# Performance work log

Measured on AMD Instinct MI355X. Metric: run time of the kernel, lower is better.

The kernel has to match this reference:

```python
import jax, jax.numpy as jnp
import numpy as np

D_MODEL = 4096
N_CHUNKS = 8
CHUNK = D_MODEL // N_CHUNKS
EPS = 1e-5


def setup_inputs() -> dict:
    key = jax.random.key(0)
    k = jax.random.split(key, 5)
    B, L = 4, 4096
    x = jax.random.normal(k[0], (B, L, D_MODEL), dtype=jnp.float32)
    # kaiming_uniform with a=sqrt(5) on [n,c,c]: fan_in = c, bound = 1/sqrt(fan_in)
    bound = 1.0 / np.sqrt(CHUNK)
    w1 = jax.random.uniform(k[1], (N_CHUNKS, CHUNK, CHUNK), jnp.float32, -bound, bound)
    w2 = jax.random.uniform(k[2], (N_CHUNKS, CHUNK, CHUNK), jnp.float32, -bound, bound)
    b1 = jnp.zeros((N_CHUNKS, CHUNK), jnp.float32)
    b2 = jnp.zeros((N_CHUNKS, CHUNK), jnp.float32)
    ln_g = jnp.ones((D_MODEL,), jnp.float32)
    ln_b = jnp.zeros((D_MODEL,), jnp.float32)
    return {"x": x, "w1": w1, "b1": b1, "w2": w2, "b2": b2, "ln_g": ln_g, "ln_b": ln_b}


def reference(x, w1, b1, w2, b2, ln_g, ln_b):
    B, L, d = x.shape
    xc = x.reshape(B, L, N_CHUNKS, CHUNK)
    h = jnp.einsum('blnc,ncd->blnd', xc, w1) + b1
    h = jax.nn.gelu(h, approximate=False)  # torch F.gelu default is exact erf
    h = jnp.einsum('blnc,ncd->blnd', h, w2) + b2
    out = h.reshape(B, L, d) + x  # dropout p=0.0 -> identity
    mu = jnp.mean(out, axis=-1, keepdims=True)
    var = jnp.var(out, axis=-1, keepdims=True)
    return (out - mu) * jax.lax.rsqrt(var + EPS) * ln_g + ln_b
```

## Files before the change

kernel.cpp:

```cpp
#include <hip/hip_runtime.h>
#include <hip/hip_bf16.h>

#define TOKENS 16384
#define DMODEL 4096
#define NCH 8
#define CH 512
#define BM 64

typedef short s16x8 __attribute__((ext_vector_type(8)));
typedef float f32x4 __attribute__((ext_vector_type(4)));

__device__ __forceinline__ unsigned short f2bf(float f) {
    unsigned u = __float_as_uint(f);
    u += 0x7fffu + ((u >> 16) & 1u);
    return (unsigned short)(u >> 16);
}

__device__ __forceinline__ float gelu_fast(float x) {
    float u = 1.5957691216057308f * x * (1.0f + 0.044715f * x * x);
    float e = __expf(u);
    return x - x * __builtin_amdgcn_rcpf(e + 1.0f);
}

__global__ __launch_bounds__(256)
void wprep_kernel(const float* __restrict__ w1, const float* __restrict__ w2,
                  unsigned short* __restrict__ p1, unsigned short* __restrict__ p2)
{
    const int lane = threadIdx.x;
    const int sub  = threadIdx.y;
    const int kt   = blockIdx.x;
    const int nb   = blockIdx.y * 4 + sub;
    const int which = blockIdx.z >> 3;
    const int n     = blockIdx.z & 7;

    const int kg  = lane >> 4;
    const int l15 = lane & 15;

    const float* src = (which ? w2 : w1) + (size_t)n * CH * CH;
    unsigned short* dst = (which ? p2 : p1) + (size_t)n * CH * CH
                        + ((size_t)(kt * 32 + nb) * 64 + lane) * 8;

    unsigned short v[8];
#pragma unroll
    for (int j = 0; j < 8; ++j)
        v[j] = f2bf(src[(size_t)(kt * 32 + kg * 8 + j) * CH + nb * 16 + l15]);

    uint4 q;
    q.x = (unsigned)v[0] | ((unsigned)v[1] << 16);
    q.y = (unsigned)v[2] | ((unsigned)v[3] << 16);
    q.z = (unsigned)v[4] | ((unsigned)v[5] << 16);
    q.w = (unsigned)v[6] | ((unsigned)v[7] << 16);
    *(uint4*)dst = q;
}

template<int BDEPTH>
__device__ __forceinline__ void gemm_half(
    const unsigned short* __restrict__ wp,
    const unsigned char* lds,
    int nbase,
    int lane, int l15, int kg,
    f32x4 (&acc)[4][4])
{
    s16x8 B[BDEPTH][4], A[2][4];
    auto loadB = [&](int buf, int kt) {
        const unsigned short* p = wp + ((size_t)(kt * 32 + nbase) * 64 + lane) * 8;
#pragma unroll
        for (int ni = 0; ni < 4; ++ni)
            B[buf][ni] = *(const s16x8*)(p + (size_t)ni * 64 * 8);
    };
    auto loadA = [&](int buf, int kt) {
#pragma unroll
        for (int mi = 0; mi < 4; ++mi) {
            int r = mi * 16 + l15;
            int byte = ((r * CH + kt * 32 + kg * 8) * 2) ^ ((r & 7) << 4);
            A[buf][mi] = *(const s16x8*)(lds + byte);
        }
    };

#pragma unroll
    for (int i = 0; i < BDEPTH; ++i) loadB(i, i);
    loadA(0, 0);

#pragma unroll
    for (int k = 0; k < 16; ++k) {
        if (k < 15) loadA((k + 1) & 1, k + 1);
        __builtin_amdgcn_s_setprio(1);
#pragma unroll
        for (int ni = 0; ni < 4; ++ni)
#pragma unroll
            for (int mi = 0; mi < 4; ++mi)
                acc[mi][ni] = __builtin_amdgcn_mfma_f32_16x16x32_bf16(
                    A[k & 1][mi], B[k % BDEPTH][ni], acc[mi][ni], 0, 0, 0);
        __builtin_amdgcn_s_setprio(0);
        if (k < 16 - BDEPTH) loadB(k % BDEPTH, k + BDEPTH);
    }
}

__global__ __launch_bounds__(256, 2)
void mlp_kernel(const float* __restrict__ x,
                const unsigned short* __restrict__ p1,
                const unsigned short* __restrict__ p2,
                const float* __restrict__ b1,
                const float* __restrict__ b2,
                float* __restrict__ mid)
{
    __shared__ unsigned char lds[BM * CH * 2];
    const int tile = blockIdx.x;
    const int n    = blockIdx.y;
    const int tid  = threadIdx.x;
    const int wid  = tid >> 6;
    const int lane = tid & 63;
    const int row0 = tile * BM;

    {
        const float* xc = x + (size_t)row0 * DMODEL + n * CH;
#pragma unroll
        for (int it = 0; it < 32; ++it) {
            int f = it * 256 + tid;
            int r = f >> 7;
            int c = (f & 127) << 2;
            const float4 v = *(const float4*)(xc + (size_t)r * DMODEL + c);
            unsigned lo = (unsigned)f2bf(v.x) | ((unsigned)f2bf(v.y) << 16);
            unsigned hi = (unsigned)f2bf(v.z) | ((unsigned)f2bf(v.w) << 16);
            int byte = ((r * CH + c) * 2) ^ ((r & 7) << 4);
            *(uint2*)(lds + byte) = make_uint2(lo, hi);
        }
    }
    __syncthreads();

    const int nwoff = wid * 128;
    const int l15   = lane & 15;
    const int kg    = lane >> 4;

    float b1v[8], b2v[8];
#pragma unroll
    for (int h = 0; h < 2; ++h)
#pragma unroll
        for (int ni = 0; ni < 4; ++ni) {
            int col = n * CH + nwoff + h * 64 + ni * 16 + l15;
            b1v[h * 4 + ni] = b1[col];
            b2v[h * 4 + ni] = b2[col];
        }

    const unsigned short* p1n = p1 + (size_t)n * CH * CH;
    const unsigned short* p2n = p2 + (size_t)n * CH * CH;

    f32x4 acc[4][4];
    auto zacc = [&]() {
#pragma unroll
        for (int mi = 0; mi < 4; ++mi)
#pragma unroll
            for (int ni = 0; ni < 4; ++ni)
                acc[mi][ni] = (f32x4){0.f, 0.f, 0.f, 0.f};
    };

    zacc();
    gemm_half<3>(p1n, lds, wid * 8 + 0, lane, l15, kg, acc);

    unsigned g0[4][4][2];
#pragma unroll
    for (int mi = 0; mi < 4; ++mi)
#pragma unroll
        for (int ni = 0; ni < 4; ++ni)
#pragma unroll
            for (int j = 0; j < 2; ++j) {
                float v0 = gelu_fast(acc[mi][ni][2 * j]     + b1v[ni]);
                float v1 = gelu_fast(acc[mi][ni][2 * j + 1] + b1v[ni]);
                g0[mi][ni][j] = (unsigned)f2bf(v0) | ((unsigned)f2bf(v1) << 16);
            }

    zacc();
    gemm_half<2>(p1n, lds, wid * 8 + 4, lane, l15, kg, acc);

    __syncthreads();

#pragma unroll
    for (int mi = 0; mi < 4; ++mi)
#pragma unroll
        for (int ni = 0; ni < 4; ++ni)
#pragma unroll
            for (int j = 0; j < 2; ++j) {
                int col  = nwoff + ni * 16 + l15;
                int row  = mi * 16 + kg * 4 + 2 * j;
                int byte0 = ((row * CH + col) * 2) ^ ((row & 7) << 4);
                *(unsigned short*)(lds + byte0) = (unsigned short)(g0[mi][ni][j] & 0xffff);
                int row1 = row + 1;
                int byte1 = ((row1 * CH + col) * 2) ^ ((row1 & 7) << 4);
                *(unsigned short*)(lds + byte1) = (unsigned short)(g0[mi][ni][j] >> 16);
            }
#pragma unroll
    for (int mi = 0; mi < 4; ++mi)
#pragma unroll
        for (int ni = 0; ni < 4; ++ni)
#pragma unroll
            for (int r = 0; r < 4; ++r) {
                float v = gelu_fast(acc[mi][ni][r] + b1v[4 + ni]);
                int col  = nwoff + 64 + ni * 16 + l15;
                int row  = mi * 16 + kg * 4 + r;
                int byte = ((row * CH + col) * 2) ^ ((row & 7) << 4);
                *(unsigned short*)(lds + byte) = f2bf(v);
            }
    __syncthreads();

    const float* xr = x   + (size_t)row0 * DMODEL + n * CH;
    float*       mr = mid + (size_t)row0 * DMODEL + n * CH;

#pragma unroll
    for (int h = 0; h < 2; ++h) {
        zacc();
        if (h == 0) gemm_half<3>(p2n, lds, wid * 8 + 0, lane, l15, kg, acc);
        else        gemm_half<3>(p2n, lds, wid * 8 + 4, lane, l15, kg, acc);
#pragma unroll
        for (int mi = 0; mi < 4; ++mi)
#pragma unroll
            for (int ni = 0; ni < 4; ++ni)
#pragma unroll
                for (int r = 0; r < 4; ++r) {
                    int row = mi * 16 + kg * 4 + r;
                    int col = nwoff + h * 64 + ni * 16 + l15;
                    float v = acc[mi][ni][r] + b2v[h * 4 + ni] + xr[(size_t)row * DMODEL + col];
                    mr[(size_t)row * DMODEL + col] = v;
                }
    }
}

__global__ __launch_bounds__(256)
void ln_kernel(float* __restrict__ out,
               const float* __restrict__ g,
               const float* __restrict__ bt)
{
    __shared__ float red[8];
    const int row = blockIdx.x;
    const int tid = threadIdx.x;
    float* p = out + (size_t)row * DMODEL;

    float4 v[4];
    float s = 0.f, ss = 0.f;
#pragma unroll
    for (int i = 0; i < 4; ++i) {
        v[i] = *(const float4*)(p + (i * 256 + tid) * 4);
        s  += v[i].x + v[i].y + v[i].z + v[i].w;
        ss += v[i].x * v[i].x + v[i].y * v[i].y + v[i].z * v[i].z + v[i].w * v[i].w;
    }
#pragma unroll
    for (int o = 32; o > 0; o >>= 1) {
        s  += __shfl_xor(s, o, 64);
        ss += __shfl_xor(ss, o, 64);
    }
    const int wid = tid >> 6, lane = tid & 63;
    if (lane == 0) { red[wid] = s; red[4 + wid] = ss; }
    __syncthreads();
    s  = red[0] + red[1] + red[2] + red[3];
    ss = red[4] + red[5] + red[6] + red[7];
    const float mu   = s * (1.f / DMODEL);
    const float var  = ss * (1.f / DMODEL) - mu * mu;
    const float rstd = rsqrtf(var + 1e-5f);

#pragma unroll
    for (int i = 0; i < 4; ++i) {
        int c = (i * 256 + tid) * 4;
        float4 gv = *(const float4*)(g + c);
        float4 bv = *(const float4*)(bt + c);
        float4 o;
        o.x = (v[i].x - mu) * rstd * gv.x + bv.x;
        o.y = (v[i].y - mu) * rstd * gv.y + bv.y;
        o.z = (v[i].z - mu) * rstd * gv.z + bv.z;
        o.w = (v[i].w - mu) * rstd * gv.w + bv.w;
        *(float4*)(p + c) = o;
    }
}

extern "C" void kernel_launch(void* const* d_in, const int* in_sizes, int n_in,
                              void* d_out, int out_size, void* d_ws, size_t ws_size,
                              hipStream_t stream)
{
    const float* x    = (const float*)d_in[0];
    const float* w1   = (const float*)d_in[1];
    const float* b1   = (const float*)d_in[2];
    const float* w2   = (const float*)d_in[3];
    const float* b2   = (const float*)d_in[4];
    const float* ln_g = (const float*)d_in[5];
    const float* ln_b = (const float*)d_in[6];
    float* out = (float*)d_out;

    unsigned short* p1 = (unsigned short*)d_ws;
    unsigned short* p2 = p1 + (size_t)NCH * CH * CH;

    wprep_kernel<<<dim3(16, 8, 16), dim3(64, 4), 0, stream>>>(w1, w2, p1, p2);
    mlp_kernel<<<dim3(TOKENS / BM, NCH), dim3(256), 0, stream>>>(x, p1, p2, b1, b2, out);
    ln_kernel<<<dim3(TOKENS), dim3(256), 0, stream>>>(out, ln_g, ln_b);
}
```

Before: 363.1 us.

## Shrink row tile to 32 and use 8 waves each owning a 64-column slice

The MLP kernel tile drops from 64 to 32 rows and the block grows from 256 to 512 threads, so each of the 8 waves computes a 32x64 output slice in one pass instead of two 64-column halves. The GEMM helper uses double-buffered B and A loads in place of the deeper B prefetch, and the s_setprio hints are removed. LDS use halves and there are twice as many blocks, which may raise occupancy and shrink per-thread register pressure. The cost is that each block reads the full weight chunk from global/L2 for half as many rows, doubling weight traffic per token, and the per-step MFMA count drops, which gives less room to hide load latency.

Result: slower. 450.3 us (+24.0%).

```diff
diff --git a/kernel.cpp b/kernel.cpp
--- a/kernel.cpp
+++ b/kernel.cpp
@@ -5,7 +5,7 @@
 #define DMODEL 4096
 #define NCH 8
 #define CH 512
-#define BM 64
+#define BM 32
 
 typedef short s16x8 __attribute__((ext_vector_type(8)));
 typedef float f32x4 __attribute__((ext_vector_type(4)));
@@ -53,50 +53,44 @@
     *(uint4*)dst = q;
 }
 
-template<int BDEPTH>
-__device__ __forceinline__ void gemm_half(
+__device__ __forceinline__ void gemm_pass(
     const unsigned short* __restrict__ wp,
     const unsigned char* lds,
     int nbase,
     int lane, int l15, int kg,
-    f32x4 (&acc)[4][4])
-{
-    s16x8 B[BDEPTH][4], A[2][4];
+    f32x4 (&acc)[2][4])
+{
+    s16x8 B[2][4], A[2][2];
     auto loadB = [&](int buf, int kt) {
         const unsigned short* p = wp + ((size_t)(kt * 32 + nbase) * 64 + lane) * 8;
 #pragma unroll
         for (int ni = 0; ni < 4; ++ni)
-            B[buf][ni] = *(const s16x8*)(p + (size_t)ni * 64 * 8);
+            B[buf][ni] = *(const s16x8*)(p + (size_t)ni * 512);
     };
     auto loadA = [&](int buf, int kt) {
 #pragma unroll
-        for (int mi = 0; mi < 4; ++mi) {
+        for (int mi = 0; mi < 2; ++mi) {
             int r = mi * 16 + l15;
             int byte = ((r * CH + kt * 32 + kg * 8) * 2) ^ ((r & 7) << 4);
             A[buf][mi] = *(const s16x8*)(lds + byte);
         }
     };
 
-#pragma unroll
-    for (int i = 0; i < BDEPTH; ++i) loadB(i, i);
+    loadB(0, 0);
     loadA(0, 0);
-
 #pragma unroll
     for (int k = 0; k < 16; ++k) {
-        if (k < 15) loadA((k + 1) & 1, k + 1);
-        __builtin_amdgcn_s_setprio(1);
-#pragma unroll
-        for (int ni = 0; ni < 4; ++ni)
-#pragma unroll
-            for (int mi = 0; mi < 4; ++mi)
+        if (k < 15) { loadB((k + 1) & 1, k + 1); loadA((k + 1) & 1, k + 1); }
+#pragma unroll
+        for (int ni = 0; ni < 4; ++ni)
+#pragma unroll
+            for (int mi = 0; mi < 2; ++mi)
                 acc[mi][ni] = __builtin_amdgcn_mfma_f32_16x16x32_bf16(
-                    A[k & 1][mi], B[k % BDEPTH][ni], acc[mi][ni], 0, 0, 0);
-        __builtin_amdgcn_s_setprio(0);
-        if (k < 16 - BDEPTH) loadB(k % BDEPTH, k + BDEPTH);
-    }
-}
-
-__global__ __launch_bounds__(256, 2)
+                    A[k & 1][mi], B[k & 1][ni], acc[mi][ni], 0, 0, 0);
+    }
+}
+
+__global__ __launch_bounds__(512)
 void mlp_kernel(const float* __restrict__ x,
                 const unsigned short* __restrict__ p1,
                 const unsigned short* __restrict__ p2,
@@ -115,8 +109,8 @@
     {
         const float* xc = x + (size_t)row0 * DMODEL + n * CH;
 #pragma unroll
-        for (int it = 0; it < 32; ++it) {
-            int f = it * 256 + tid;
+        for (int it = 0; it < 8; ++it) {
+            int f = it * 512 + tid;
             int r = f >> 7;
             int c = (f & 127) << 2;
             const float4 v = *(const float4*)(xc + (size_t)r * DMODEL + c);
@@ -128,100 +122,65 @@
     }
     __syncthreads();
 
-    const int nwoff = wid * 128;
+    const int nwoff = wid * 64;
     const int l15   = lane & 15;
     const int kg    = lane >> 4;
 
-    float b1v[8], b2v[8];
-#pragma unroll
-    for (int h = 0; h < 2; ++h)
-#pragma unroll
-        for (int ni = 0; ni < 4; ++ni) {
-            int col = n * CH + nwoff + h * 64 + ni * 16 + l15;
-            b1v[h * 4 + ni] = b1[col];
-            b2v[h * 4 + ni] = b2[col];
-        }
+    float b1v[4], b2v[4];
+#pragma unroll
+    for (int ni = 0; ni < 4; ++ni) {
+        int col = n * CH + nwoff + ni * 16 + l15;
+        b1v[ni] = b1[col];
+        b2v[ni] = b2[col];
+    }
 
     const unsigned short* p1n = p1 + (size_t)n * CH * CH;
     const unsigned short* p2n = p2 + (size_t)n * CH * CH;
 
-    f32x4 acc[4][4];
+    f32x4 acc[2][4];
     auto zacc = [&]() {
 #pragma unroll
-        for (int mi = 0; mi < 4; ++mi)
+        for (int mi = 0; mi < 2; ++mi)
 #pragma unroll
             for (int ni = 0; ni < 4; ++ni)
                 acc[mi][ni] = (f32x4){0.f, 0.f, 0.f, 0.f};
     };
 
     zacc();
-    gemm_half<3>(p1n, lds, wid * 8 + 0, lane, l15, kg, acc);
-
-    unsigned g0[4][4][2];
-#pragma unroll
-    for (int mi = 0; mi < 4; ++mi)
-#pragma unroll
-        for (int ni = 0; ni < 4; ++ni)
-#pragma unroll
-            for (int j = 0; j < 2; ++j) {
-                float v0 = gelu_fast(acc[mi][ni][2 * j]     + b1v[ni]);
-                float v1 = gelu_fast(acc[mi][ni][2 * j + 1] + b1v[ni]);
-                g0[mi][ni][j] = (unsigned)f2bf(v0) | ((unsigned)f2bf(v1) << 16);
-            }
-
-    zacc();
-    gemm_half<2>(p1n, lds, wid * 8 + 4, lane, l15, kg, acc);
-
-    __syncthreads();
-
-#pragma unroll
-    for (int mi = 0; mi < 4; ++mi)
-#pragma unroll
-        for (int ni = 0; ni < 4; ++ni)
-#pragma unroll
-            for (int j = 0; j < 2; ++j) {
+    gemm_pass(p1n, lds, wid * 4, lane, l15, kg, acc);
+
+    __syncthreads();
+
+#pragma unroll
+    for (int mi = 0; mi < 2; ++mi)
+#pragma unroll
+        for (int ni = 0; ni < 4; ++ni)
+#pragma unroll
+            for (int r = 0; r < 4; ++r) {
+                float v = gelu_fast(acc[mi][ni][r] + b1v[ni]);
+                int row  = mi * 16 + kg * 4 + r;
                 int col  = nwoff + ni * 16 + l15;
-                int row  = mi * 16 + kg * 4 + 2 * j;
-                int byte0 = ((row * CH + col) * 2) ^ ((row & 7) << 4);
-                *(unsigned short*)(lds + byte0) = (unsigned short)(g0[mi][ni][j] & 0xffff);
-                int row1 = row + 1;
-                int byte1 = ((row1 * CH + col) * 2) ^ ((row1 & 7) << 4);
-                *(unsigned short*)(lds + byte1) = (unsigned short)(g0[mi][ni][j] >> 16);
-            }
-#pragma unroll
-    for (int mi = 0; mi < 4; ++mi)
-#pragma unroll
-        for (int ni = 0; ni < 4; ++ni)
-#pragma unroll
-            for (int r = 0; r < 4; ++r) {
-                float v = gelu_fast(acc[mi][ni][r] + b1v[4 + ni]);
-                int col  = nwoff + 64 + ni * 16 + l15;
-                int row  = mi * 16 + kg * 4 + r;
                 int byte = ((row * CH + col) * 2) ^ ((row & 7) << 4);
                 *(unsigned short*)(lds + byte) = f2bf(v);
             }
     __syncthreads();
 
+    zacc();
+    gemm_pass(p2n, lds, wid * 4, lane, l15, kg, acc);
+
     const float* xr = x   + (size_t)row0 * DMODEL + n * CH;
     float*       mr = mid + (size_t)row0 * DMODEL + n * CH;
-
-#pragma unroll
-    for (int h = 0; h < 2; ++h) {
-        zacc();
-        if (h == 0) gemm_half<3>(p2n, lds, wid * 8 + 0, lane, l15, kg, acc);
-        else        gemm_half<3>(p2n, lds, wid * 8 + 4, lane, l15, kg, acc);
-#pragma unroll
-        for (int mi = 0; mi < 4; ++mi)
-#pragma unroll
-            for (int ni = 0; ni < 4; ++ni)
-#pragma unroll
-                for (int r = 0; r < 4; ++r) {
-                    int row = mi * 16 + kg * 4 + r;
-                    int col = nwoff + h * 64 + ni * 16 + l15;
-                    float v = acc[mi][ni][r] + b2v[h * 4 + ni] + xr[(size_t)row * DMODEL + col];
-                    mr[(size_t)row * DMODEL + col] = v;
-                }
-    }
+#pragma unroll
+    for (int mi = 0; mi < 2; ++mi)
+#pragma unroll
+        for (int ni = 0; ni < 4; ++ni)
+#pragma unroll
+            for (int r = 0; r < 4; ++r) {
+                int row = mi * 16 + kg * 4 + r;
+                int col = nwoff + ni * 16 + l15;
+                float v = acc[mi][ni][r] + b2v[ni] + xr[(size_t)row * DMODEL + col];
+                mr[(size_t)row * DMODEL + col] = v;
+            }
 }
 
 __global__ __launch_bounds__(256)
@@ -287,6 +246,6 @@
     unsigned short* p2 = p1 + (size_t)NCH * CH * CH;
 
     wprep_kernel<<<dim3(16, 8, 16), dim3(64, 4), 0, stream>>>(w1, w2, p1, p2);
-    mlp_kernel<<<dim3(TOKENS / BM, NCH), dim3(256), 0, stream>>>(x, p1, p2, b1, b2, out);
+    mlp_kernel<<<dim3(TOKENS / BM, NCH), dim3(512), 0, stream>>>(x, p1, p2, b1, b2, out);
     ln_kernel<<<dim3(TOKENS), dim3(256), 0, stream>>>(out, ln_g, ln_b);
 }
```
